# Optimization experiments

Measured on AMD Instinct MI355X. Metric: run time of the kernel, lower is better.

The kernel has to match this reference:

```python
import jax, jax.numpy as jnp
import numpy as np

N = 200000
C = 128
VOX = 0.05
EPS = 1e-5
OFFSETS = np.array([[dz, dy, dx] for dz in (-1, 0, 1) for dy in (-1, 0, 1) for dx in (-1, 0, 1)], dtype=np.int64)


def setup_inputs() -> dict:
    key = jax.random.key(0)
    ks = jax.random.split(key, 8)
    gp = jax.random.normal(ks[0], (N, 14), jnp.float32)
    # ---- voxelization tables (int constants, computed once in numpy) ----
    pts = np.asarray(gp[:, :3], dtype=np.float64)
    vc = np.floor(pts / VOX).astype(np.int64)
    vc = vc - vc.min(axis=0)
    mx = vc.max(axis=0) + 1
    h = vc[:, 0] * mx[1] * mx[2] + vc[:, 1] * mx[2] + vc[:, 2]
    uh, inv = np.unique(h, return_inverse=True)
    M = int(uh.shape[0])
    vcoord = np.zeros((M, 3), np.int64)
    vcoord[inv] = vc  # coords identical for same hash
    nbr_idx = np.zeros((M, 27), np.int32)
    nbr_mask = np.zeros((M, 27), np.float32)
    for o in range(27):
        nc = vcoord + OFFSETS[o]
        inb = (nc >= 0).all(1) & (nc < mx).all(1)
        nh = nc[:, 0] * mx[1] * mx[2] + nc[:, 1] * mx[2] + nc[:, 2]
        pos = np.clip(np.searchsorted(uh, nh), 0, M - 1)
        found = inb & (uh[pos] == nh)
        nbr_idx[:, o] = np.where(found, pos, 0)
        nbr_mask[:, o] = found.astype(np.float32)
    s = 0.05
    return {
        'gaussian_params': gp,
        'w_enc': jax.random.normal(ks[1], (14, C), jnp.float32) * s,
        'b_enc': jnp.zeros((C,), jnp.float32),
        'ln_g': jnp.ones((C,), jnp.float32),
        'ln_b': jnp.zeros((C,), jnp.float32),
        'conv_w': jax.random.normal(ks[2], (4, 27, C, C), jnp.float32) * s,
        'bn_g': jnp.ones((4, C), jnp.float32),
        'bn_b': jnp.zeros((4, C), jnp.float32),
        'w1': jax.random.normal(ks[3], (C, C // 2), jnp.float32) * s,
        'b1': jnp.zeros((C // 2,), jnp.float32),
        'w2': jax.random.normal(ks[4], (C // 2, 14), jnp.float32) * s,
        'b2': jnp.zeros((14,), jnp.float32),
        'nbr_mask': jnp.asarray(nbr_mask),
        'inv_idx': jnp.asarray(inv.astype(np.int32)),
        'nbr_idx': jnp.asarray(nbr_idx),
        'num_voxels': M,
    }


def _bn(x, g, b):
    m = x.mean(0)
    v = x.var(0)
    return (x - m) * jax.lax.rsqrt(v + EPS) * g + b


def _subm(x, W, nbr_idx, nbr_mask):
    # submanifold 3x3x3 conv: sum over 27 offsets of masked neighbor gather @ W[o]
    out = jnp.zeros_like(x)
    for o in range(27):
        out = out + (x[nbr_idx[:, o]] * nbr_mask[:, o:o + 1]) @ W[o]
    return out


def _forward(gp, w_enc, b_enc, ln_g, ln_b, conv_w, bn_g, bn_b, w1, b1, w2, b2, nbr_mask, inv_idx, nbr_idx, num_voxels):
    # input encoder: Linear -> LayerNorm -> ReLU
    f = gp @ w_enc + b_enc
    mu = f.mean(-1, keepdims=True)
    var = f.var(-1, keepdims=True)
    f = jax.nn.relu((f - mu) * jax.lax.rsqrt(var + EPS) * ln_g + ln_b)
    # points -> voxels: segment mean (the op the torch code did with a Python loop)
    cnt = jax.ops.segment_sum(jnp.ones((gp.shape[0],), f.dtype), inv_idx, num_segments=num_voxels)
    x = jax.ops.segment_sum(f, inv_idx, num_segments=num_voxels) / cnt[:, None]
    # 2 residual sparse conv blocks (BN uses batch stats, training-mode forward)
    for blk in range(2):
        idn = x
        out = _subm(x, conv_w[2 * blk], nbr_idx, nbr_mask)
        out = jax.nn.relu(_bn(out, bn_g[2 * blk], bn_b[2 * blk]))
        out = _subm(out, conv_w[2 * blk + 1], nbr_idx, nbr_mask)
        x = jax.nn.relu(_bn(out, bn_g[2 * blk + 1], bn_b[2 * blk + 1]) + idn)
    # voxels -> points, output head, residual add
    pf = x[inv_idx]
    delta = jax.nn.relu(pf @ w1 + b1) @ w2 + b2
    return gp[:, :14] + delta


def reference(gaussian_params, w_enc, b_enc, ln_g, ln_b, conv_w, bn_g, bn_b, w1, b1, w2, b2, nbr_mask, inv_idx, nbr_idx, num_voxels):
    return _forward(gaussian_params, w_enc, b_enc, ln_g, ln_b, conv_w, bn_g, bn_b, w1, b1, w2, b2, nbr_mask, inv_idx, nbr_idx, num_voxels)
```

## Files before the change

### kernel.cpp

```cpp
#include <hip/hip_runtime.h>

typedef __bf16 bf16x8 __attribute__((ext_vector_type(8)));
typedef float f32x16 __attribute__((ext_vector_type(16)));

#define LN_EPS 1e-5f

__device__ __forceinline__ unsigned f2bf_rne(float f) {
    unsigned x = __float_as_uint(f);
    return (x + 0x7fffu + ((x >> 16) & 1u)) >> 16;
}

__device__ __forceinline__ float bf2f(unsigned short u) {
    return __uint_as_float((unsigned)u << 16);
}

__global__ void pack_w_kernel(const float* __restrict__ cw, unsigned short* __restrict__ Wp, int E) {
    int idx = blockIdx.x * 256 + threadIdx.x;
    if (idx >= E) return;
    float v = cw[idx];
    int n  = idx & 127;
    int c  = (idx >> 7) & 127;
    int oc = idx >> 14;
    Wp[oc * 16384 + (c >> 3) * 1024 + n * 8 + (c & 7)] = (unsigned short)f2bf_rne(v);
}

__global__ void pack_w1_kernel(const float* __restrict__ w1, unsigned short* __restrict__ Wp1) {
    int idx = blockIdx.x * 256 + threadIdx.x;
    if (idx >= 8192) return;
    int k = idx >> 6, n = idx & 63;
    Wp1[(k >> 3) * 512 + n * 8 + (k & 7)] = (unsigned short)f2bf_rne(w1[k * 64 + n]);
}

__global__ void prep_nbr_kernel(const int* __restrict__ nbr_idx, const float* __restrict__ nbr_mask,
                                int* __restrict__ T, unsigned* __restrict__ act64, int M) {
    int m = blockIdx.x * 256 + threadIdx.x;
    if (m >= M) return;
    unsigned bits = 0;
#pragma unroll
    for (int o = 0; o < 27; ++o) {
        bool f = nbr_mask[m * 27 + o] != 0.f;
        int g = f ? nbr_idx[m * 27 + o] : M;
        T[o * M + m] = g;
        bits |= (f ? 1u : 0u) << o;
    }
    atomicOr(&act64[m >> 6], bits);
}

__global__ __launch_bounds__(256) void encode_kernel(
    const float* __restrict__ gp, const float* __restrict__ w_enc,
    const float* __restrict__ b_enc, const float* __restrict__ ln_g,
    const float* __restrict__ ln_b, const int* __restrict__ inv_idx,
    float* __restrict__ vsum, float* __restrict__ cnt, int N)
{
    int p = blockIdx.x * 4 + (threadIdx.x >> 6);
    int lane = threadIdx.x & 63;
    if (p >= N) return;
    float gv[14];
#pragma unroll
    for (int i = 0; i < 14; ++i) gv[i] = gp[p * 14 + i];
    float f0 = b_enc[lane], f1 = b_enc[lane + 64];
#pragma unroll
    for (int i = 0; i < 14; ++i) {
        f0 = fmaf(gv[i], w_enc[i * 128 + lane], f0);
        f1 = fmaf(gv[i], w_enc[i * 128 + lane + 64], f1);
    }
    float s = f0 + f1;
#pragma unroll
    for (int off = 32; off; off >>= 1) s += __shfl_xor(s, off);
    float mean = s * 0.0078125f;
    float d0 = f0 - mean, d1 = f1 - mean;
    float v = d0 * d0 + d1 * d1;
#pragma unroll
    for (int off = 32; off; off >>= 1) v += __shfl_xor(v, off);
    float rs = rsqrtf(v * 0.0078125f + LN_EPS);
    float h0 = d0 * rs * ln_g[lane] + ln_b[lane];
    float h1 = d1 * rs * ln_g[lane + 64] + ln_b[lane + 64];
    h0 = h0 > 0.f ? h0 : 0.f;
    h1 = h1 > 0.f ? h1 : 0.f;
    int vx = inv_idx[p];
    atomicAdd(&vsum[vx * 128 + lane], h0);
    atomicAdd(&vsum[vx * 128 + lane + 64], h1);
    if (lane == 0) atomicAdd(&cnt[vx], 1.0f);
}

__global__ void vox_mean_kernel(const float* __restrict__ vsum, const float* __restrict__ cnt,
                                unsigned short* __restrict__ out, int total4) {
    int idx = blockIdx.x * 256 + threadIdx.x;
    if (idx >= total4) return;
    int e0 = idx * 4;
    float r = 1.f / cnt[e0 >> 7];
    float4 v = *(const float4*)(vsum + e0);
    uint2 pk;
    pk.x = f2bf_rne(v.x * r) | (f2bf_rne(v.y * r) << 16);
    pk.y = f2bf_rne(v.z * r) | (f2bf_rne(v.w * r) << 16);
    *(uint2*)(out + e0) = pk;
}

__global__ __launch_bounds__(256) void subm_conv_kernel(
    const unsigned short* __restrict__ xin,
    const unsigned short* __restrict__ Wp,
    const int* __restrict__ T, const unsigned* __restrict__ act64,
    float* __restrict__ yout, float* __restrict__ stats, int M)
{
    const int tid = threadIdx.x;
    const int lane = tid & 63;
    const int w = tid >> 6;

    const int nwg = gridDim.x;
    const int orig = blockIdx.x;
    const int xcd = orig & 7;
    const int q8 = nwg >> 3, r8 = nwg & 7;
    const int tile = (xcd < r8 ? xcd * (q8 + 1) : r8 * (q8 + 1) + (xcd - r8) * q8) + (orig >> 3);

    const int m0 = tile * 256;
    const int rw = w * 64;
    const int q = lane >> 5;
    const int l31 = lane & 31;
    int row0 = m0 + rw + l31;
    int row1 = row0 + 32;
    if (row0 >= M) row0 = M - 1;
    if (row1 >= M) row1 = M - 1;

    f32x16 acc0[4], acc1[4];
#pragma unroll
    for (int t = 0; t < 4; ++t)
#pragma unroll
        for (int r = 0; r < 16; ++r) { acc0[t][r] = 0.f; acc1[t][r] = 0.f; }

    const uint4* xin4 = (const uint4*)xin;
    const bf16x8* WpB = (const bf16x8*)Wp;

    unsigned amask = act64[tile * 4 + w];

    if (amask) {
        int o = __ffs(amask) - 1; amask &= amask - 1;
        int h0 = T[o * M + row0], h1 = T[o * M + row1];
        uint4 af0[8], af1[8];
#pragma unroll
        for (int j = 0; j < 8; ++j) {
            af0[j] = xin4[h0 * 16 + 2 * j + q];
            af1[j] = xin4[h1 * 16 + 2 * j + q];
        }
        int o1 = -1;
        if (amask) {
            o1 = __ffs(amask) - 1; amask &= amask - 1;
            h0 = T[o1 * M + row0]; h1 = T[o1 * M + row1];
        }

        const bf16x8* Bo = WpB + (size_t)o * 2048;
        bf16x8 bp[4][4];
#pragma unroll
        for (int s = 0; s < 3; ++s) {
            int kb = (s << 1) | q;
            bp[s][0] = Bo[kb * 128 + l31];
            bp[s][1] = Bo[kb * 128 + 32 + l31];
            bp[s][2] = Bo[kb * 128 + 64 + l31];
            bp[s][3] = Bo[kb * 128 + 96 + l31];
        }

        while (true) {
            int o2 = -1, i0 = 0, i1 = 0;
            if (amask) {
                o2 = __ffs(amask) - 1; amask &= amask - 1;
                i0 = T[o2 * M + row0]; i1 = T[o2 * M + row1];
            }

            const bool more = (o1 >= 0);
            const bf16x8* Bn = WpB + (size_t)(more ? o1 : o) * 2048;

            __builtin_amdgcn_s_setprio(1);
#pragma unroll
            for (int ks = 0; ks < 8; ++ks) {
                const int cs = ks & 3;
                const int ls = (ks + 3) & 3;
                bf16x8 bc0 = bp[cs][0], bc1 = bp[cs][1], bc2 = bp[cs][2], bc3 = bp[cs][3];
                if (ks < 5) {
                    int kb = ((ks + 3) << 1) | q;
                    bp[ls][0] = Bo[kb * 128 + l31];
                    bp[ls][1] = Bo[kb * 128 + 32 + l31];
                    bp[ls][2] = Bo[kb * 128 + 64 + l31];
                    bp[ls][3] = Bo[kb * 128 + 96 + l31];
                } else if (more) {
                    int kb = ((ks - 5) << 1) | q;
                    bp[ls][0] = Bn[kb * 128 + l31];
                    bp[ls][1] = Bn[kb * 128 + 32 + l31];
                    bp[ls][2] = Bn[kb * 128 + 64 + l31];
                    bp[ls][3] = Bn[kb * 128 + 96 + l31];
                }
                bf16x8 a0 = *(const bf16x8*)&af0[ks];
                bf16x8 a1 = *(const bf16x8*)&af1[ks];
                if (more) {
                    af0[ks] = xin4[h0 * 16 + 2 * ks + q];
                    af1[ks] = xin4[h1 * 16 + 2 * ks + q];
                }
                acc0[0] = __builtin_amdgcn_mfma_f32_32x32x16_bf16(a0, bc0, acc0[0], 0, 0, 0);
                acc1[0] = __builtin_amdgcn_mfma_f32_32x32x16_bf16(a1, bc0, acc1[0], 0, 0, 0);
                acc0[1] = __builtin_amdgcn_mfma_f32_32x32x16_bf16(a0, bc1, acc0[1], 0, 0, 0);
                acc1[1] = __builtin_amdgcn_mfma_f32_32x32x16_bf16(a1, bc1, acc1[1], 0, 0, 0);
                acc0[2] = __builtin_amdgcn_mfma_f32_32x32x16_bf16(a0, bc2, acc0[2], 0, 0, 0);
                acc1[2] = __builtin_amdgcn_mfma_f32_32x32x16_bf16(a1, bc2, acc1[2], 0, 0, 0);
                acc0[3] = __builtin_amdgcn_mfma_f32_32x32x16_bf16(a0, bc3, acc0[3], 0, 0, 0);
                acc1[3] = __builtin_amdgcn_mfma_f32_32x32x16_bf16(a1, bc3, acc1[3], 0, 0, 0);
            }
            __builtin_amdgcn_s_setprio(0);

            if (!more) break;
            o = o1; o1 = o2; h0 = i0; h1 = i1;
            Bo = Bn;
        }
    }

#pragma unroll
    for (int tn = 0; tn < 4; ++tn) {
        int col = tn * 32 + l31;
        float s = 0.f, sq = 0.f;
#pragma unroll
        for (int r = 0; r < 16; ++r) {
            int rloc = (r & 3) + 8 * (r >> 2) + 4 * q + rw;
            int grow = m0 + rloc;
            float v = (grow < M) ? acc0[tn][r] : 0.f;
            if (grow < M) yout[grow * 128 + col] = v;
            s += v; sq += v * v;
        }
#pragma unroll
        for (int r = 0; r < 16; ++r) {
            int rloc = (r & 3) + 8 * (r >> 2) + 4 * q + rw + 32;
            int grow = m0 + rloc;
            float v = (grow < M) ? acc1[tn][r] : 0.f;
            if (grow < M) yout[grow * 128 + col] = v;
            s += v; sq += v * v;
        }
        s += __shfl_xor(s, 32);
        sq += __shfl_xor(sq, 32);
        if (lane < 32) {
            atomicAdd(&stats[col], s);
            atomicAdd(&stats[128 + col], sq);
        }
    }
}

__global__ void bn_relu_kernel(const float* __restrict__ y, const float* __restrict__ stats,
                               const float* __restrict__ g, const float* __restrict__ b,
                               unsigned short* __restrict__ out, int total4, float invM) {
    int idx = blockIdx.x * 256 + threadIdx.x;
    if (idx >= total4) return;
    int e0 = idx * 4;
    int c0 = e0 & 127;
    float4 yv = *(const float4*)(y + e0);
    float h[4];
    const float* yp = (const float*)&yv;
#pragma unroll
    for (int j = 0; j < 4; ++j) {
        int c = c0 + j;
        float mean = stats[c] * invM;
        float var = stats[128 + c] * invM - mean * mean;
        float sc = g[c] * rsqrtf(var + LN_EPS);
        float sh = b[c] - mean * sc;
        float vv = yp[j] * sc + sh;
        h[j] = vv > 0.f ? vv : 0.f;
    }
    uint2 pk;
    pk.x = f2bf_rne(h[0]) | (f2bf_rne(h[1]) << 16);
    pk.y = f2bf_rne(h[2]) | (f2bf_rne(h[3]) << 16);
    *(uint2*)(out + e0) = pk;
}

__global__ void bn_relu_res_kernel(const float* __restrict__ y, const float* __restrict__ stats,
                                   const float* __restrict__ g, const float* __restrict__ b,
                                   const unsigned short* __restrict__ idn,
                                   unsigned short* __restrict__ out, int total4, float invM) {
    int idx = blockIdx.x * 256 + threadIdx.x;
    if (idx >= total4) return;
    int e0 = idx * 4;
    int c0 = e0 & 127;
    float4 yv = *(const float4*)(y + e0);
    uint2 iv = *(const uint2*)(idn + e0);
    float id[4];
    id[0] = __uint_as_float(iv.x << 16);
    id[1] = __uint_as_float(iv.x & 0xffff0000u);
    id[2] = __uint_as_float(iv.y << 16);
    id[3] = __uint_as_float(iv.y & 0xffff0000u);
    float h[4];
    const float* yp = (const float*)&yv;
#pragma unroll
    for (int j = 0; j < 4; ++j) {
        int c = c0 + j;
        float mean = stats[c] * invM;
        float var = stats[128 + c] * invM - mean * mean;
        float sc = g[c] * rsqrtf(var + LN_EPS);
        float sh = b[c] - mean * sc;
        float vv = yp[j] * sc + sh + id[j];
        h[j] = vv > 0.f ? vv : 0.f;
    }
    uint2 pk;
    pk.x = f2bf_rne(h[0]) | (f2bf_rne(h[1]) << 16);
    pk.y = f2bf_rne(h[2]) | (f2bf_rne(h[3]) << 16);
    *(uint2*)(out + e0) = pk;
}

__global__ __launch_bounds__(256) void head_vox_kernel(
    const unsigned short* __restrict__ A,
    const unsigned short* __restrict__ Wp1,
    const float* __restrict__ b1, const float* __restrict__ w2,
    const float* __restrict__ b2, float* __restrict__ Dv, int M)
{
    __shared__ uint4 W1s[1024];
    __shared__ unsigned short Hs[8192];
    __shared__ float w2s[896];

    const int tid = threadIdx.x;
    const int lane = tid & 63;
    const int w = tid >> 6;
    const int m0 = blockIdx.x * 128;
    const int rw = w * 32;
    const int q = lane >> 5;
    const int l31 = lane & 31;
    int myrow = m0 + rw + l31;
    if (myrow > M) myrow = M;

    for (int i = tid; i < 1024; i += 256) W1s[i] = ((const uint4*)Wp1)[i];
    for (int i = tid; i < 896; i += 256) w2s[i] = w2[i];

    const uint4* xin4 = (const uint4*)A;
    uint4 af[8];
#pragma unroll
    for (int j = 0; j < 8; ++j) af[j] = xin4[myrow * 16 + 2 * j + q];

    f32x16 acc[2];
#pragma unroll
    for (int t = 0; t < 2; ++t)
#pragma unroll
        for (int r = 0; r < 16; ++r) acc[t][r] = 0.f;

    __syncthreads();

#pragma unroll
    for (int ks = 0; ks < 8; ++ks) {
        int kb = (ks << 1) | q;
        bf16x8 a = *(const bf16x8*)&af[ks];
#pragma unroll
        for (int tn = 0; tn < 2; ++tn) {
            bf16x8 b = ((const bf16x8*)W1s)[kb * 64 + tn * 32 + l31];
            acc[tn] = __builtin_amdgcn_mfma_f32_32x32x16_bf16(a, b, acc[tn], 0, 0, 0);
        }
    }

#pragma unroll
    for (int tn = 0; tn < 2; ++tn) {
        int col = tn * 32 + l31;
        float bias = b1[col];
        int ch = col >> 3, ce = col & 7;
#pragma unroll
        for (int r = 0; r < 16; ++r) {
            int rloc = (r & 3) + 8 * (r >> 2) + 4 * q + rw;
            float v = acc[tn][r] + bias;
            v = v > 0.f ? v : 0.f;
            Hs[rloc * 64 + (ch ^ (rloc & 7)) * 8 + ce] = (unsigned short)f2bf_rne(v);
        }
    }
    __syncthreads();

    int r2 = tid >> 1;
    int c0 = (tid & 1) * 7;
    float o[7];
#pragma unroll
    for (int j = 0; j < 7; ++j) o[j] = b2[c0 + j];
#pragma unroll
    for (int c = 0; c < 8; ++c) {
        bf16x8 hv = ((const bf16x8*)Hs)[r2 * 8 + (c ^ (r2 & 7))];
#pragma unroll
        for (int e = 0; e < 8; ++e) {
            float h = bf2f(((const unsigned short*)&hv)[e]);
            int k = c * 8 + e;
#pragma unroll
            for (int j = 0; j < 7; ++j) o[j] = fmaf(h, w2s[k * 14 + c0 + j], o[j]);
        }
    }
    int grow = m0 + r2;
    if (grow < M) {
#pragma unroll
        for (int j = 0; j < 7; ++j) Dv[grow * 14 + c0 + j] = o[j];
    }
}

__global__ void head_scatter_kernel(const float* __restrict__ gp, const float* __restrict__ Dv,
                                    const int* __restrict__ inv_idx, float* __restrict__ out, int N) {
    int p = blockIdx.x * 256 + threadIdx.x;
    if (p >= N) return;
    int vx = inv_idx[p];
#pragma unroll
    for (int c = 0; c < 14; ++c) out[p * 14 + c] = gp[p * 14 + c] + Dv[vx * 14 + c];
}

extern "C" void kernel_launch(void* const* d_in, const int* in_sizes, int n_in,
                              void* d_out, int out_size, void* d_ws, size_t ws_size,
                              hipStream_t stream) {
    const float* gp       = (const float*)d_in[0];
    const float* w_enc    = (const float*)d_in[1];
    const float* b_enc    = (const float*)d_in[2];
    const float* ln_g     = (const float*)d_in[3];
    const float* ln_b     = (const float*)d_in[4];
    const float* conv_w   = (const float*)d_in[5];
    const float* bn_g     = (const float*)d_in[6];
    const float* bn_b     = (const float*)d_in[7];
    const float* w1       = (const float*)d_in[8];
    const float* b1       = (const float*)d_in[9];
    const float* w2       = (const float*)d_in[10];
    const float* b2       = (const float*)d_in[11];
    const float* nbr_mask = (const float*)d_in[12];
    const int*   inv_idx  = (const int*)d_in[13];
    const int*   nbr_idx  = (const int*)d_in[14];

    const int N = in_sizes[0] / 14;
    const int M = in_sizes[12] / 27;
    const int ntiles = (M + 127) / 128;
    const int ntiles256 = (M + 255) / 256;

    char* ws = (char*)d_ws;
    size_t off = 0;
    unsigned short* Wp = (unsigned short*)(ws + off); off += (size_t)4 * 27 * 16384 * 2;
    unsigned short* A  = (unsigned short*)(ws + off); off += (size_t)(M + 1) * 128 * 2;
    unsigned short* H  = (unsigned short*)(ws + off); off += (size_t)(M + 1) * 128 * 2;
    float* Yraw  = (float*)(ws + off);
    size_t zoff = off;
    off += (size_t)M * 128 * 4;
    float* cnt   = (float*)(ws + off); off += (size_t)M * 4;
    float* stats = (float*)(ws + off); off += 4 * 256 * 4;
    unsigned* act64 = (unsigned*)(ws + off); off += (size_t)ntiles256 * 4 * 4;
    size_t zbytes = off - zoff;
    int* T = (int*)(ws + off); off += (size_t)27 * M * 4;
    unsigned short* Wp1 = (unsigned short*)(ws + off); off += 8192 * 2;
    float* Dv = Yraw;

    hipMemsetAsync(Yraw, 0, zbytes, stream);
    hipMemsetAsync(A + (size_t)M * 128, 0, 256, stream);
    hipMemsetAsync(H + (size_t)M * 128, 0, 256, stream);

    const int E = 4 * 27 * 128 * 128;
    pack_w_kernel<<<(E + 255) / 256, 256, 0, stream>>>(conv_w, Wp, E);
    pack_w1_kernel<<<32, 256, 0, stream>>>(w1, Wp1);
    prep_nbr_kernel<<<(M + 255) / 256, 256, 0, stream>>>(nbr_idx, nbr_mask, T, act64, M);
    encode_kernel<<<(N + 3) / 4, 256, 0, stream>>>(gp, w_enc, b_enc, ln_g, ln_b, inv_idx, Yraw, cnt, N);
    const int total4 = M * 32;
    vox_mean_kernel<<<(total4 + 255) / 256, 256, 0, stream>>>(Yraw, cnt, A, total4);

    const float invM = 1.f / (float)M;
    for (int blk = 0; blk < 2; ++blk) {
        int c0 = 2 * blk, c1 = 2 * blk + 1;
        subm_conv_kernel<<<ntiles256, 256, 0, stream>>>(
            A, Wp + (size_t)c0 * 27 * 16384, T, act64, Yraw, stats + c0 * 256, M);
        bn_relu_kernel<<<(total4 + 255) / 256, 256, 0, stream>>>(
            Yraw, stats + c0 * 256, bn_g + c0 * 128, bn_b + c0 * 128, H, total4, invM);
        subm_conv_kernel<<<ntiles256, 256, 0, stream>>>(
            H, Wp + (size_t)c1 * 27 * 16384, T, act64, Yraw, stats + c1 * 256, M);
        bn_relu_res_kernel<<<(total4 + 255) / 256, 256, 0, stream>>>(
            Yraw, stats + c1 * 256, bn_g + c1 * 128, bn_b + c1 * 128, A, A, total4, invM);
    }
    head_vox_kernel<<<ntiles, 256, 0, stream>>>(A, Wp1, b1, w2, b2, Dv, M);
    head_scatter_kernel<<<(N + 255) / 256, 256, 0, stream>>>(gp, Dv, inv_idx, (float*)d_out, N);
}
```

Baseline: 1.383 ms.

## Stage gathered neighbor rows into LDS via async global_load_lds double buffering

Replaces the per-lane register gather of neighbor feature rows with direct global-to-LDS async loads (global_load_lds) into a per-wave double buffer with an XOR swizzle. Each offset's rows are staged one iteration ahead and then read from LDS into registers before the MFMA loop. The cross-iteration prefetch of weights is dropped, so weights for each offset are now loaded at the start of the iteration. The aim is to cut register pressure and improve gather coalescing. In exchange it adds a full vmcnt(0) wait per offset and 128KB of LDS per block, which limits occupancy to one block per CU (launch bounds set accordingly).

Measured after the change: 1.921 ms. 38.9% more time.

```diff
diff --git a/kernel.cpp b/kernel.cpp
--- a/kernel.cpp
+++ b/kernel.cpp
@@ -4,6 +4,8 @@
 typedef float f32x16 __attribute__((ext_vector_type(16)));
 
 #define LN_EPS 1e-5f
+#define AS1 __attribute__((address_space(1)))
+#define AS3 __attribute__((address_space(3)))
 
 __device__ __forceinline__ unsigned f2bf_rne(float f) {
     unsigned x = __float_as_uint(f);
@@ -96,12 +98,14 @@
     *(uint2*)(out + e0) = pk;
 }
 
-__global__ __launch_bounds__(256) void subm_conv_kernel(
+__global__ __launch_bounds__(256, 1) void subm_conv_kernel(
     const unsigned short* __restrict__ xin,
     const unsigned short* __restrict__ Wp,
     const int* __restrict__ T, const unsigned* __restrict__ act64,
     float* __restrict__ yout, float* __restrict__ stats, int M)
 {
+    __shared__ uint4 Abuf[8192];
+
     const int tid = threadIdx.x;
     const int lane = tid & 63;
     const int w = tid >> 6;
@@ -116,10 +120,10 @@
     const int rw = w * 64;
     const int q = lane >> 5;
     const int l31 = lane & 31;
-    int row0 = m0 + rw + l31;
-    int row1 = row0 + 32;
-    if (row0 >= M) row0 = M - 1;
-    if (row1 >= M) row1 = M - 1;
+    const int wbase = w * 2048;
+
+    int rowt = m0 + rw + lane;
+    if (rowt >= M) rowt = M - 1;
 
     f32x16 acc0[4], acc1[4];
 #pragma unroll
@@ -132,41 +136,59 @@
 
     unsigned amask = act64[tile * 4 + w];
 
+#define STAGE_A(TV, BUFSEL)                                                           \
+    _Pragma("unroll")                                                                 \
+    for (int j = 0; j < 16; ++j) {                                                    \
+        int rloc = 4 * j + (lane >> 4);                                               \
+        int g = __shfl((TV), rloc);                                                   \
+        int csrc = (lane & 15) ^ (rloc & 7);                                          \
+        __builtin_amdgcn_global_load_lds(                                             \
+            (const AS1 unsigned int*)(xin4 + (size_t)g * 16 + csrc),                  \
+            (AS3 unsigned int*)(Abuf + wbase + (BUFSEL) * 1024 + j * 64), 16, 0, 0);  \
+    }
+
     if (amask) {
         int o = __ffs(amask) - 1; amask &= amask - 1;
-        int h0 = T[o * M + row0], h1 = T[o * M + row1];
-        uint4 af0[8], af1[8];
-#pragma unroll
-        for (int j = 0; j < 8; ++j) {
-            af0[j] = xin4[h0 * 16 + 2 * j + q];
-            af1[j] = xin4[h1 * 16 + 2 * j + q];
-        }
-        int o1 = -1;
+        int tcur = T[o * M + rowt];
+        STAGE_A(tcur, 0);
+        int o1 = -1, t1 = 0;
         if (amask) {
             o1 = __ffs(amask) - 1; amask &= amask - 1;
-            h0 = T[o1 * M + row0]; h1 = T[o1 * M + row1];
-        }
-
-        const bf16x8* Bo = WpB + (size_t)o * 2048;
-        bf16x8 bp[4][4];
-#pragma unroll
-        for (int s = 0; s < 3; ++s) {
-            int kb = (s << 1) | q;
-            bp[s][0] = Bo[kb * 128 + l31];
-            bp[s][1] = Bo[kb * 128 + 32 + l31];
-            bp[s][2] = Bo[kb * 128 + 64 + l31];
-            bp[s][3] = Bo[kb * 128 + 96 + l31];
-        }
+            t1 = T[o1 * M + rowt];
+        }
+        int buf = 0;
 
         while (true) {
-            int o2 = -1, i0 = 0, i1 = 0;
+            asm volatile("s_waitcnt vmcnt(0)" ::: "memory");
+
+            int o2 = -1, t2 = 0;
             if (amask) {
                 o2 = __ffs(amask) - 1; amask &= amask - 1;
-                i0 = T[o2 * M + row0]; i1 = T[o2 * M + row1];
+                t2 = T[o2 * M + rowt];
             }
-
             const bool more = (o1 >= 0);
-            const bf16x8* Bn = WpB + (size_t)(more ? o1 : o) * 2048;
+
+            if (more) STAGE_A(t1, buf ^ 1);
+
+            const bf16x8* Bo = WpB + (size_t)o * 2048;
+            bf16x8 bp[4][4];
+#pragma unroll
+            for (int s = 0; s < 3; ++s) {
+                int kb = (s << 1) | q;
+                bp[s][0] = Bo[kb * 128 + l31];
+                bp[s][1] = Bo[kb * 128 + 32 + l31];
+                bp[s][2] = Bo[kb * 128 + 64 + l31];
+                bp[s][3] = Bo[kb * 128 + 96 + l31];
+            }
+
+            const bf16x8* Ab = (const bf16x8*)(Abuf + wbase + buf * 1024);
+            bf16x8 af0[8], af1[8];
+#pragma unroll
+            for (int ks = 0; ks < 8; ++ks) {
+                int c = (2 * ks + q) ^ (l31 & 7);
+                af0[ks] = Ab[l31 * 16 + c];
+                af1[ks] = Ab[(32 + l31) * 16 + c];
+            }
 
             __builtin_amdgcn_s_setprio(1);
 #pragma unroll
@@ -180,35 +202,23 @@
                     bp[ls][1] = Bo[kb * 128 + 32 + l31];
                     bp[ls][2] = Bo[kb * 128 + 64 + l31];
                     bp[ls][3] = Bo[kb * 128 + 96 + l31];
-                } else if (more) {
-                    int kb = ((ks - 5) << 1) | q;
-                    bp[ls][0] = Bn[kb * 128 + l31];
-                    bp[ls][1] = Bn[kb * 128 + 32 + l31];
-                    bp[ls][2] = Bn[kb * 128 + 64 + l31];
-                    bp[ls][3] = Bn[kb * 128 + 96 + l31];
                 }
-                bf16x8 a0 = *(const bf16x8*)&af0[ks];
-                bf16x8 a1 = *(const bf16x8*)&af1[ks];
-                if (more) {
-                    af0[ks] = xin4[h0 * 16 + 2 * ks + q];
-                    af1[ks] = xin4[h1 * 16 + 2 * ks + q];
-                }
-                acc0[0] = __builtin_amdgcn_mfma_f32_32x32x16_bf16(a0, bc0, acc0[0], 0, 0, 0);
-                acc1[0] = __builtin_amdgcn_mfma_f32_32x32x16_bf16(a1, bc0, acc1[0], 0, 0, 0);
-                acc0[1] = __builtin_amdgcn_mfma_f32_32x32x16_bf16(a0, bc1, acc0[1], 0, 0, 0);
-                acc1[1] = __builtin_amdgcn_mfma_f32_32x32x16_bf16(a1, bc1, acc1[1], 0, 0, 0);
-                acc0[2] = __builtin_amdgcn_mfma_f32_32x32x16_bf16(a0, bc2, acc0[2], 0, 0, 0);
-                acc1[2] = __builtin_amdgcn_mfma_f32_32x32x16_bf16(a1, bc2, acc1[2], 0, 0, 0);
-                acc0[3] = __builtin_amdgcn_mfma_f32_32x32x16_bf16(a0, bc3, acc0[3], 0, 0, 0);
-                acc1[3] = __builtin_amdgcn_mfma_f32_32x32x16_bf16(a1, bc3, acc1[3], 0, 0, 0);
+                acc0[0] = __builtin_amdgcn_mfma_f32_32x32x16_bf16(af0[ks], bc0, acc0[0], 0, 0, 0);
+                acc1[0] = __builtin_amdgcn_mfma_f32_32x32x16_bf16(af1[ks], bc0, acc1[0], 0, 0, 0);
+                acc0[1] = __builtin_amdgcn_mfma_f32_32x32x16_bf16(af0[ks], bc1, acc0[1], 0, 0, 0);
+                acc1[1] = __builtin_amdgcn_mfma_f32_32x32x16_bf16(af1[ks], bc1, acc1[1], 0, 0, 0);
+                acc0[2] = __builtin_amdgcn_mfma_f32_32x32x16_bf16(af0[ks], bc2, acc0[2], 0, 0, 0);
+                acc1[2] = __builtin_amdgcn_mfma_f32_32x32x16_bf16(af1[ks], bc2, acc1[2], 0, 0, 0);
+                acc0[3] = __builtin_amdgcn_mfma_f32_32x32x16_bf16(af0[ks], bc3, acc0[3], 0, 0, 0);
+                acc1[3] = __builtin_amdgcn_mfma_f32_32x32x16_bf16(af1[ks], bc3, acc1[3], 0, 0, 0);
             }
             __builtin_amdgcn_s_setprio(0);
 
             if (!more) break;
-            o = o1; o1 = o2; h0 = i0; h1 = i1;
-            Bo = Bn;
-        }
-    }
+            o = o1; o1 = o2; t1 = t2; buf ^= 1;
+        }
+    }
+#undef STAGE_A
 
 #pragma unroll
     for (int tn = 0; tn < 4; ++tn) {
```
